# Kernel tuning notes

Measured on AMD Instinct MI355X. Metric: run time of the kernel, lower is better.

The kernel has to match this reference:

```python
import jax, jax.numpy as jnp
import numpy as np

N_NODES = 100000


def _gcn_conv(h, src, dst, norm, W, b):
    # h: [N, F_in] -> [N, F_out]; aggregate normalized messages over edges
    h = h @ W                                   # transform first (cheaper messages)
    msg = h[src] * norm[:, None]                # [E_tot, F_out]
    agg = jax.ops.segment_sum(msg, dst, num_segments=N_NODES)
    return agg + b


def setup_inputs() -> dict:
    key = jax.random.key(0)
    k1, k2, k3, k4 = jax.random.split(key, 4)
    x = jax.random.normal(k1, (N_NODES, 256), dtype=jnp.float32)
    edge_index = jax.random.randint(k2, (2, 1600000), 0, N_NODES, dtype=jnp.int64)
    W1 = jax.random.normal(k3, (256, 128), dtype=jnp.float32) * (1.0 / np.sqrt(256))
    b1 = jnp.zeros((128,), dtype=jnp.float32)
    W2 = jax.random.normal(k4, (128, 40), dtype=jnp.float32) * (1.0 / np.sqrt(128))
    b2 = jnp.zeros((40,), dtype=jnp.float32)
    return {"x": x, "edge_index": edge_index, "W1": W1, "b1": b1, "W2": W2, "b2": b2}


def reference(x, edge_index, W1, b1, W2, b2):
    # add self-loops
    loop = jnp.arange(N_NODES, dtype=edge_index.dtype)
    src = jnp.concatenate([edge_index[0], loop])
    dst = jnp.concatenate([edge_index[1], loop])
    # symmetric normalization D^{-1/2} (A+I) D^{-1/2}
    deg = jax.ops.segment_sum(jnp.ones_like(dst, dtype=x.dtype), dst, num_segments=N_NODES)
    dinv = jax.lax.rsqrt(jnp.maximum(deg, 1.0))
    norm = dinv[src] * dinv[dst]                # [E_tot]

    h = _gcn_conv(x, src, dst, norm, W1, b1)
    h = jax.nn.relu(h)                          # dropout p=0 / eval -> identity
    h = _gcn_conv(h, src, dst, norm, W2, b2)
    return jax.nn.log_softmax(h, axis=1)
```

## Files before the change

### kernel.cpp

```cpp
#include <hip/hip_runtime.h>
#include <hip/hip_fp8.h>
#include <math.h>

#define N_NODES 100000
#define N_EDGES 1600000
#define F_IN 256
#define F_H 128
#define F_OUT 40

#define BIN_SHIFT 9
#define BIN_NODES 512
#define NBIN 196
#define CAP 12288
#define CNT_PAD 16
#define PART_CHUNK 8192

typedef __attribute__((ext_vector_type(8))) short bf16x8;
typedef __attribute__((ext_vector_type(4))) float floatx4;
typedef __attribute__((ext_vector_type(2))) float floatx2;
typedef __attribute__((ext_vector_type(2))) unsigned int uintx2;

__device__ __forceinline__ unsigned short f2bf(float f) {
    unsigned int u = __float_as_uint(f);
    u += 0x7fffu + ((u >> 16) & 1u);
    return (unsigned short)(u >> 16);
}
__device__ __forceinline__ float bf2f(unsigned short s) { return __uint_as_float(((unsigned int)s) << 16); }

#if defined(__has_builtin)
#if __has_builtin(__builtin_amdgcn_cvt_pk_fp8_f32)
#define HAVE_PK_ENC 1
#endif
#if __has_builtin(__builtin_amdgcn_cvt_pk_f32_fp8)
#define HAVE_PK_DEC 1
#endif
#if __has_builtin(__builtin_amdgcn_cvt_f32_fp8)
#define HAVE_SC_DEC 1
#endif
#endif

__device__ __forceinline__ unsigned char f2f8(float f) {
#ifdef HAVE_PK_ENC
    int r = __builtin_amdgcn_cvt_pk_fp8_f32(f, f, 0, false);
    return (unsigned char)(r & 0xff);
#else
    __hip_fp8_e4m3 t(f);
    return (unsigned char)t.__x;
#endif
}
__device__ __forceinline__ float f82f(unsigned char b) {
#ifdef HAVE_SC_DEC
    return __builtin_amdgcn_cvt_f32_fp8((int)b, 0);
#else
    __hip_fp8_e4m3 t; t.__x = (__hip_fp8_storage_t)b;
    return (float)t;
#endif
}
__device__ __forceinline__ floatx2 f8x2tof(unsigned short u) {
#ifdef HAVE_PK_DEC
    return __builtin_amdgcn_cvt_pk_f32_fp8((int)u, false);
#else
    floatx2 r;
    r.x = f82f((unsigned char)(u & 0xff));
    r.y = f82f((unsigned char)(u >> 8));
    return r;
#endif
}

__global__ void k_zero(int* p, int n) {
    int i = blockIdx.x * blockDim.x + threadIdx.x;
    if (i < n) p[i] = 0;
}

__global__ __launch_bounds__(256) void k_part(const int* __restrict__ eidx,
                                              int* __restrict__ gcnt,
                                              unsigned int* __restrict__ parts) {
    __shared__ int hist[4][NBIN];
    __shared__ int sbase[NBIN];
    __shared__ int rcnt[NBIN];
    const int tid = threadIdx.x;
    const int wv = tid >> 6;
    for (int i = tid; i < NBIN; i += 256) {
        hist[0][i] = 0; hist[1][i] = 0; hist[2][i] = 0; hist[3][i] = 0; rcnt[i] = 0;
    }
    __syncthreads();
    const int e0 = blockIdx.x * PART_CHUNK;
    const int e1 = min(e0 + PART_CHUNK, N_EDGES);
    for (int e = e0 + tid; e < e1; e += 256) {
        int d = eidx[N_EDGES + e];
        atomicAdd(&hist[wv][d >> BIN_SHIFT], 1);
    }
    __syncthreads();
    for (int b = tid; b < NBIN; b += 256) {
        int tot = hist[0][b] + hist[1][b] + hist[2][b] + hist[3][b];
        int old = atomicAdd(&gcnt[b * CNT_PAD], tot);
        sbase[b] = b * CAP + old;
    }
    __syncthreads();
    for (int e = e0 + tid; e < e1; e += 256) {
        int d = eidx[N_EDGES + e];
        int s = eidx[e];
        int b = d >> BIN_SHIFT;
        int r = atomicAdd(&rcnt[b], 1);
        parts[sbase[b] + r] = ((unsigned int)s << BIN_SHIFT) | (unsigned int)(d & (BIN_NODES - 1));
    }
}

__global__ __launch_bounds__(256) void k_build(const unsigned int* __restrict__ parts,
                                               const int* __restrict__ gcnt,
                                               int* __restrict__ rowptr,
                                               float* __restrict__ dinv,
                                               int* __restrict__ csr_src) {
    __shared__ int deg[4][BIN_NODES];
    __shared__ int cur[BIN_NODES];
    __shared__ int scan[256];
    const int tid = threadIdx.x;
    const int wv = tid >> 6;
    const int g = blockIdx.x;

    scan[tid] = (tid < NBIN) ? gcnt[tid * CNT_PAD] : 0;
    __syncthreads();
    for (int off = 1; off < 256; off <<= 1) {
        int v = 0;
        if (tid >= off) v = scan[tid - off];
        __syncthreads();
        if (tid >= off) scan[tid] += v;
        __syncthreads();
    }
    const int binBase = (g == 0) ? 0 : scan[g - 1];
    const int cntg = scan[g] - binBase;

    for (int i = tid; i < BIN_NODES; i += 256) {
        deg[0][i] = 0; deg[1][i] = 0; deg[2][i] = 0; deg[3][i] = 0;
    }
    __syncthreads();

    const unsigned int* pp = parts + (size_t)g * CAP;
    for (int i = tid; i < cntg; i += 256)
        atomicAdd(&deg[wv][pp[i] & (BIN_NODES - 1)], 1);
    __syncthreads();

    const int n0 = 2 * tid, n1 = 2 * tid + 1;
    const int d0 = deg[0][n0] + deg[1][n0] + deg[2][n0] + deg[3][n0];
    const int d1 = deg[0][n1] + deg[1][n1] + deg[2][n1] + deg[3][n1];
    scan[tid] = d0 + d1;
    __syncthreads();
    for (int off = 1; off < 256; off <<= 1) {
        int v = 0;
        if (tid >= off) v = scan[tid - off];
        __syncthreads();
        if (tid >= off) scan[tid] += v;
        __syncthreads();
    }
    const int pre = (tid == 0) ? 0 : scan[tid - 1];
    const int p0 = binBase + pre;
    const int p1 = p0 + d0;
    const int node0 = g * BIN_NODES + n0;
    if (node0 < N_NODES)     { rowptr[node0]     = p0; dinv[node0]     = rsqrtf((float)d0 + 1.0f); }
    if (node0 + 1 < N_NODES) { rowptr[node0 + 1] = p1; dinv[node0 + 1] = rsqrtf((float)d1 + 1.0f); }
    cur[n0] = p0;
    cur[n1] = p1;
    __syncthreads();

    for (int i = tid; i < cntg; i += 256) {
        unsigned int u = pp[i];
        int pos = atomicAdd(&cur[u & (BIN_NODES - 1)], 1);
        csr_src[pos] = (int)(u >> BIN_SHIFT);
    }
    if (g == NBIN - 1 && tid == 0) rowptr[N_NODES] = N_EDGES;
}

__global__ void k_cvt_w(const float* __restrict__ W1, const float* __restrict__ W2,
                        short* __restrict__ W1t, short* __restrict__ W2t) {
    int b = blockIdx.x, t = threadIdx.x;
    if (b < 128) {
        int idx = b * 256 + t;
        int n = idx >> 8, k = idx & 255;
        W1t[n * 256 + k] = (short)f2bf(W1[k * 128 + n]);
    } else {
        int idx = (b - 128) * 256 + t;
        if (idx < 48 * 128) {
            int n = idx >> 7, k = idx & 127;
            float v = (n < F_OUT) ? W2[k * F_OUT + n] : 0.f;
            W2t[n * 128 + k] = (short)f2bf(v);
        }
    }
}

__global__ __launch_bounds__(256) void k_gemm1_mfma(const float* __restrict__ x,
                                                    const short* __restrict__ W1t,
                                                    const float* __restrict__ dinv,
                                                    unsigned char* __restrict__ h1f8) {
    __shared__ short As[128 * 40];
    __shared__ short Bs[128 * 264];
    __shared__ float Ds[128];
    const int tid = threadIdx.x;
    const int row0 = blockIdx.x * 128;
    const int w = tid >> 6, l = tid & 63;
    const int l15 = l & 15, q = l >> 4;
    const int ar = tid >> 1;
    const int ak = (tid & 1) * 16;

    {
        const int n = tid >> 1;
        const int kh = (tid & 1) * 128;
#pragma unroll
        for (int i = 0; i < 16; ++i)
            *(bf16x8*)&Bs[n * 264 + kh + i * 8] = *(const bf16x8*)&W1t[n * 256 + kh + i * 8];
    }
    if (tid < 128) {
        int r = row0 + tid;
        Ds[tid] = (r < N_NODES) ? dinv[r] : 0.f;
    }

    floatx4 acc[2][8];
#pragma unroll
    for (int a = 0; a < 2; ++a)
#pragma unroll
        for (int nt = 0; nt < 8; ++nt) acc[a][nt] = (floatx4)0.f;

    const bool arow_ok = (row0 + ar) < N_NODES;
    const float* xp = x + (size_t)(row0 + ar) * F_IN;

    for (int k0 = 0; k0 < F_IN; k0 += 32) {
        bf16x8 av0 = (bf16x8)0, av1 = (bf16x8)0;
        if (arow_ok) {
            floatx4 f0 = *(const floatx4*)(xp + k0 + ak);
            floatx4 f1 = *(const floatx4*)(xp + k0 + ak + 4);
            floatx4 f2 = *(const floatx4*)(xp + k0 + ak + 8);
            floatx4 f3 = *(const floatx4*)(xp + k0 + ak + 12);
            av0[0] = (short)f2bf(f0[0]); av0[1] = (short)f2bf(f0[1]);
            av0[2] = (short)f2bf(f0[2]); av0[3] = (short)f2bf(f0[3]);
            av0[4] = (short)f2bf(f1[0]); av0[5] = (short)f2bf(f1[1]);
            av0[6] = (short)f2bf(f1[2]); av0[7] = (short)f2bf(f1[3]);
            av1[0] = (short)f2bf(f2[0]); av1[1] = (short)f2bf(f2[1]);
            av1[2] = (short)f2bf(f2[2]); av1[3] = (short)f2bf(f2[3]);
            av1[4] = (short)f2bf(f3[0]); av1[5] = (short)f2bf(f3[1]);
            av1[6] = (short)f2bf(f3[2]); av1[7] = (short)f2bf(f3[3]);
        }
        __syncthreads();
        *(bf16x8*)&As[ar * 40 + ak]     = av0;
        *(bf16x8*)&As[ar * 40 + ak + 8] = av1;
        __syncthreads();

        bf16x8 af[2], bfr[8];
#pragma unroll
        for (int a = 0; a < 2; ++a)
            af[a] = *(const bf16x8*)&As[((w * 2 + a) * 16 + l15) * 40 + q * 8];
#pragma unroll
        for (int nt = 0; nt < 8; ++nt)
            bfr[nt] = *(const bf16x8*)&Bs[(nt * 16 + l15) * 264 + k0 + q * 8];
#pragma unroll
        for (int a = 0; a < 2; ++a)
#pragma unroll
            for (int nt = 0; nt < 8; ++nt)
                acc[a][nt] = __builtin_amdgcn_mfma_f32_16x16x32_bf16(af[a], bfr[nt], acc[a][nt], 0, 0, 0);
    }
#pragma unroll
    for (int a = 0; a < 2; ++a) {
#pragma unroll
        for (int r = 0; r < 4; ++r) {
            const int rl = (w * 2 + a) * 16 + q * 4 + r;
            const int row = row0 + rl;
            if (row < N_NODES) {
                const float ds = Ds[rl];
                unsigned char* hp = h1f8 + (size_t)row * F_H;
#pragma unroll
                for (int nt = 0; nt < 8; ++nt)
                    hp[nt * 16 + l15] = f2f8(acc[a][nt][r] * ds);
            }
        }
    }
}

__global__ __launch_bounds__(256) void k_spmm1(const int* __restrict__ rowptr,
                                               const int* __restrict__ csr_src,
                                               const unsigned int* __restrict__ h1d,
                                               const float* __restrict__ dinv,
                                               const float* __restrict__ b1,
                                               uintx2* __restrict__ agg1p2) {
    const int half = threadIdx.x >> 5;
    const int p = threadIdx.x & 31;
    int node = blockIdx.x * 8 + half;
    bool valid = node < N_NODES;
    int nd = valid ? node : 0;
    int beg = rowptr[nd];
    int end = valid ? rowptr[nd + 1] : beg;
    float dv = dinv[nd];

    unsigned int su = h1d[(size_t)nd * 32 + p];
    floatx2 s01 = f8x2tof((unsigned short)(su & 0xffffu));
    floatx2 s23 = f8x2tof((unsigned short)(su >> 16));
    float A0 = s01.x, A1 = s01.y, A2 = s23.x, A3 = s23.y;
    float B0 = 0.f, B1 = 0.f, B2 = 0.f, B3 = 0.f;
    float C0 = 0.f, C1 = 0.f, C2 = 0.f, C3 = 0.f;
    float D0 = 0.f, D1 = 0.f, D2 = 0.f, D3 = 0.f;

    int i = beg;
    for (; i + 3 < end; i += 4) {
        int s0 = csr_src[i], s1 = csr_src[i + 1], s2 = csr_src[i + 2], s3 = csr_src[i + 3];
        unsigned int u0 = h1d[(size_t)s0 * 32 + p];
        unsigned int u1 = h1d[(size_t)s1 * 32 + p];
        unsigned int u2 = h1d[(size_t)s2 * 32 + p];
        unsigned int u3 = h1d[(size_t)s3 * 32 + p];
        floatx2 a01 = f8x2tof((unsigned short)(u0 & 0xffffu));
        floatx2 a23 = f8x2tof((unsigned short)(u0 >> 16));
        floatx2 b01 = f8x2tof((unsigned short)(u1 & 0xffffu));
        floatx2 b23 = f8x2tof((unsigned short)(u1 >> 16));
        floatx2 c01 = f8x2tof((unsigned short)(u2 & 0xffffu));
        floatx2 c23 = f8x2tof((unsigned short)(u2 >> 16));
        floatx2 d01 = f8x2tof((unsigned short)(u3 & 0xffffu));
        floatx2 d23 = f8x2tof((unsigned short)(u3 >> 16));
        A0 += a01.x; A1 += a01.y; A2 += a23.x; A3 += a23.y;
        B0 += b01.x; B1 += b01.y; B2 += b23.x; B3 += b23.y;
        C0 += c01.x; C1 += c01.y; C2 += c23.x; C3 += c23.y;
        D0 += d01.x; D1 += d01.y; D2 += d23.x; D3 += d23.y;
    }
    for (; i < end; ++i) {
        unsigned int u0 = h1d[(size_t)csr_src[i] * 32 + p];
        floatx2 a01 = f8x2tof((unsigned short)(u0 & 0xffffu));
        floatx2 a23 = f8x2tof((unsigned short)(u0 >> 16));
        A0 += a01.x; A1 += a01.y; A2 += a23.x; A3 += a23.y;
    }

    float4 bb = *(const float4*)&b1[4 * p];
    float v0 = fmaf((A0 + B0) + (C0 + D0), dv, bb.x);
    float v1 = fmaf((A1 + B1) + (C1 + D1), dv, bb.y);
    float v2 = fmaf((A2 + B2) + (C2 + D2), dv, bb.z);
    float v3 = fmaf((A3 + B3) + (C3 + D3), dv, bb.w);
    v0 = v0 > 0.f ? v0 : 0.f;
    v1 = v1 > 0.f ? v1 : 0.f;
    v2 = v2 > 0.f ? v2 : 0.f;
    v3 = v3 > 0.f ? v3 : 0.f;
    if (valid) {
        uintx2 o;
        o.x = ((unsigned int)f2bf(v1) << 16) | f2bf(v0);
        o.y = ((unsigned int)f2bf(v3) << 16) | f2bf(v2);
        agg1p2[(size_t)node * 32 + p] = o;
    }
}

__global__ __launch_bounds__(256) void k_gemm2_mfma(const unsigned short* __restrict__ agg1b,
                                                    const short* __restrict__ W2t,
                                                    const float* __restrict__ dinv,
                                                    unsigned char* __restrict__ h2f8) {
    __shared__ short As[128 * 40];
    __shared__ short Bs[48 * 136];
    __shared__ float Ds[128];
    const int tid = threadIdx.x;
    const int row0 = blockIdx.x * 128;
    const int w = tid >> 6, l = tid & 63;
    const int l15 = l & 15, q = l >> 4;
    const int ar = tid >> 1;
    const int ak = (tid & 1) * 16;

#pragma unroll
    for (int i = 0; i < 3; ++i) {
        int c = tid * 3 + i;
        int n = c >> 4, koff = (c & 15) * 8;
        *(bf16x8*)&Bs[n * 136 + koff] = *(const bf16x8*)&W2t[n * 128 + koff];
    }
    if (tid < 128) {
        int r = row0 + tid;
        Ds[tid] = (r < N_NODES) ? dinv[r] : 0.f;
    }

    floatx4 acc[2][3];
#pragma unroll
    for (int a = 0; a < 2; ++a)
#pragma unroll
        for (int nt = 0; nt < 3; ++nt) acc[a][nt] = (floatx4)0.f;

    const bool arow_ok = (row0 + ar) < N_NODES;
    const unsigned short* ap = agg1b + (size_t)(row0 + ar) * F_H;

    for (int k0 = 0; k0 < F_H; k0 += 32) {
        bf16x8 a0, a1;
        if (arow_ok) {
            a0 = *(const bf16x8*)(ap + k0 + ak);
            a1 = *(const bf16x8*)(ap + k0 + ak + 8);
        } else {
            a0 = (bf16x8)0; a1 = (bf16x8)0;
        }
        *(bf16x8*)&As[ar * 40 + ak]     = a0;
        *(bf16x8*)&As[ar * 40 + ak + 8] = a1;
        __syncthreads();

        bf16x8 af[2], bfr[3];
#pragma unroll
        for (int a = 0; a < 2; ++a)
            af[a] = *(const bf16x8*)&As[((w * 2 + a) * 16 + l15) * 40 + q * 8];
#pragma unroll
        for (int nt = 0; nt < 3; ++nt)
            bfr[nt] = *(const bf16x8*)&Bs[(nt * 16 + l15) * 136 + k0 + q * 8];
#pragma unroll
        for (int a = 0; a < 2; ++a)
#pragma unroll
            for (int nt = 0; nt < 3; ++nt)
                acc[a][nt] = __builtin_amdgcn_mfma_f32_16x16x32_bf16(af[a], bfr[nt], acc[a][nt], 0, 0, 0);
        __syncthreads();
    }
#pragma unroll
    for (int a = 0; a < 2; ++a) {
#pragma unroll
        for (int nt = 0; nt < 3; ++nt) {
            int col = nt * 16 + l15;
#pragma unroll
            for (int r = 0; r < 4; ++r) {
                int rl = (w * 2 + a) * 16 + q * 4 + r;
                int row = row0 + rl;
                if (row < N_NODES && col < F_OUT)
                    h2f8[(size_t)row * F_OUT + col] = f2f8(acc[a][nt][r] * Ds[rl]);
            }
        }
    }
}

__global__ __launch_bounds__(256) void k_spmm2_lsm(const int* __restrict__ rowptr,
                                                   const int* __restrict__ csr_src,
                                                   const unsigned int* __restrict__ h2d,
                                                   const float* __restrict__ dinv,
                                                   const float* __restrict__ b2,
                                                   float* __restrict__ out) {
    const int qid = threadIdx.x >> 4;
    const int p = threadIdx.x & 15;
    int node = blockIdx.x * 16 + qid;
    bool nvalid = node < N_NODES;
    bool valid = nvalid && (p < 10);
    int nd = nvalid ? node : 0;
    int beg = 0, end = 0;
    if (valid) { beg = rowptr[nd]; end = rowptr[nd + 1]; }
    float dv = dinv[nd];

    float A0 = 0.f, A1 = 0.f, A2 = 0.f, A3 = 0.f;
    float B0 = 0.f, B1 = 0.f, B2 = 0.f, B3 = 0.f;
    if (valid) {
        unsigned int su = h2d[(size_t)nd * 10 + p];
        floatx2 t0 = f8x2tof((unsigned short)(su & 0xffffu));
        floatx2 t1 = f8x2tof((unsigned short)(su >> 16));
        A0 = t0.x; A1 = t0.y; A2 = t1.x; A3 = t1.y;
    }
    int i = beg;
    for (; i + 1 < end; i += 2) {
        int s0 = csr_src[i], s1 = csr_src[i + 1];
        unsigned int u0 = h2d[(size_t)s0 * 10 + p];
        unsigned int u1 = h2d[(size_t)s1 * 10 + p];
        floatx2 a01 = f8x2tof((unsigned short)(u0 & 0xffffu));
        floatx2 a23 = f8x2tof((unsigned short)(u0 >> 16));
        floatx2 b01 = f8x2tof((unsigned short)(u1 & 0xffffu));
        floatx2 b23 = f8x2tof((unsigned short)(u1 >> 16));
        A0 += a01.x; A1 += a01.y; A2 += a23.x; A3 += a23.y;
        B0 += b01.x; B1 += b01.y; B2 += b23.x; B3 += b23.y;
    }
    if (i < end) {
        unsigned int u0 = h2d[(size_t)csr_src[i] * 10 + p];
        floatx2 a01 = f8x2tof((unsigned short)(u0 & 0xffffu));
        floatx2 a23 = f8x2tof((unsigned short)(u0 >> 16));
        A0 += a01.x; A1 += a01.y; A2 += a23.x; A3 += a23.y;
    }

    float v0 = -INFINITY, v1 = -INFINITY, v2 = -INFINITY, v3 = -INFINITY;
    if (valid) {
        float4 bb = *(const float4*)&b2[4 * p];
        v0 = fmaf(A0 + B0, dv, bb.x);
        v1 = fmaf(A1 + B1, dv, bb.y);
        v2 = fmaf(A2 + B2, dv, bb.z);
        v3 = fmaf(A3 + B3, dv, bb.w);
    }
    float m = fmaxf(fmaxf(v0, v1), fmaxf(v2, v3));
#pragma unroll
    for (int off = 1; off < 16; off <<= 1) m = fmaxf(m, __shfl_xor(m, off, 16));
    float e = 0.f;
    if (valid) e = expf(v0 - m) + expf(v1 - m) + expf(v2 - m) + expf(v3 - m);
#pragma unroll
    for (int off = 1; off < 16; off <<= 1) e += __shfl_xor(e, off, 16);
    if (valid) {
        float ls = logf(e);
        floatx4 o;
        o[0] = v0 - m - ls; o[1] = v1 - m - ls; o[2] = v2 - m - ls; o[3] = v3 - m - ls;
        __builtin_nontemporal_store(o, (floatx4*)&out[(size_t)node * F_OUT + 4 * p]);
    }
}

extern "C" void kernel_launch(void* const* d_in, const int* in_sizes, int n_in,
                              void* d_out, int out_size, void* d_ws, size_t ws_size,
                              hipStream_t stream) {
    const float* x = (const float*)d_in[0];
    const int* eidx = (const int*)d_in[1];
    const float* W1 = (const float*)d_in[2];
    const float* b1 = (const float*)d_in[3];
    const float* W2 = (const float*)d_in[4];
    const float* b2 = (const float*)d_in[5];
    float* out = (float*)d_out;

    char* ws = (char*)d_ws;
    int*   gcnt      = (int*)  (ws);
    int*   rowptr    = (int*)  (ws + 400512);
    int*   csr_src   = (int*)  (ws + 1200528);
    float* dinv      = (float*)(ws + 7600528);
    short* W1t       = (short*)(ws + 8000528);
    short* W2t       = (short*)(ws + 8066064);
    unsigned char*  h1f8  = (unsigned char*) (ws + 8078352);
    unsigned short* agg1b = (unsigned short*)(ws + 20878352);
    unsigned int*   parts = (unsigned int*)  (ws + 20878352);
    unsigned char*  h2f8  = (unsigned char*) (ws + 46478352);

    k_zero<<<(NBIN * CNT_PAD + 255) / 256, 256, 0, stream>>>(gcnt, NBIN * CNT_PAD);
    k_part<<<(N_EDGES + PART_CHUNK - 1) / PART_CHUNK, 256, 0, stream>>>(eidx, gcnt, parts);
    k_build<<<NBIN, 256, 0, stream>>>(parts, gcnt, rowptr, dinv, csr_src);

    k_cvt_w<<<152, 256, 0, stream>>>(W1, W2, W1t, W2t);

    k_gemm1_mfma<<<(N_NODES + 127) / 128, 256, 0, stream>>>(x, W1t, dinv, h1f8);
    k_spmm1<<<(N_NODES + 7) / 8, 256, 0, stream>>>(rowptr, csr_src,
                                                   (const unsigned int*)h1f8, dinv, b1,
                                                   (uintx2*)agg1b);
    k_gemm2_mfma<<<(N_NODES + 127) / 128, 256, 0, stream>>>(agg1b, W2t, dinv, h2f8);
    k_spmm2_lsm<<<(N_NODES + 15) / 16, 256, 0, stream>>>(rowptr, csr_src,
                                                         (const unsigned int*)h2f8, dinv, b2, out);
}
```

Baseline: 339.7 us.

## Widen SpMM1 gathers to 16-byte loads and remap blocks for XCD locality

k_spmm1 now uses 8 lanes per node, each loading 16 fp8 features as one 128-bit vector, in place of 32 lanes loading 4 bytes each. Outputs are written as two 128-bit stores. Block IDs in both k_spmm1 and k_gemm2 are remapped so that consecutive node ranges go to the same XCD (blockIdx mod 8), which should improve L2 reuse between dependent kernels. Each thread now holds 32 accumulators, which raises register pressure, and the remap hardcodes the grid sizes and N_NODES.

```diff
diff --git a/kernel.cpp b/kernel.cpp
--- a/kernel.cpp
+++ b/kernel.cpp
@@ -19,6 +19,7 @@
 typedef __attribute__((ext_vector_type(4))) float floatx4;
 typedef __attribute__((ext_vector_type(2))) float floatx2;
 typedef __attribute__((ext_vector_type(2))) unsigned int uintx2;
+typedef __attribute__((ext_vector_type(4))) unsigned int uintx4;
 
 __device__ __forceinline__ unsigned short f2bf(float f) {
     unsigned int u = __float_as_uint(f);
@@ -65,6 +66,16 @@
     r.y = f82f((unsigned char)(u >> 8));
     return r;
 #endif
+}
+
+__device__ __forceinline__ void acc16(uintx4 u, float* a) {
+#pragma unroll
+    for (int d = 0; d < 4; ++d) {
+        floatx2 lo = f8x2tof((unsigned short)(u[d] & 0xffffu));
+        floatx2 hi = f8x2tof((unsigned short)(u[d] >> 16));
+        a[d * 4 + 0] += lo.x; a[d * 4 + 1] += lo.y;
+        a[d * 4 + 2] += hi.x; a[d * 4 + 3] += hi.y;
+    }
 }
 
 __global__ void k_zero(int* p, int n) {
@@ -275,69 +286,55 @@
 
 __global__ __launch_bounds__(256) void k_spmm1(const int* __restrict__ rowptr,
                                                const int* __restrict__ csr_src,
-                                               const unsigned int* __restrict__ h1d,
+                                               const uintx4* __restrict__ h1d4,
                                                const float* __restrict__ dinv,
                                                const float* __restrict__ b1,
-                                               uintx2* __restrict__ agg1p2) {
-    const int half = threadIdx.x >> 5;
-    const int p = threadIdx.x & 31;
-    int node = blockIdx.x * 8 + half;
-    bool valid = node < N_NODES;
-    int nd = valid ? node : 0;
-    int beg = rowptr[nd];
-    int end = valid ? rowptr[nd + 1] : beg;
-    float dv = dinv[nd];
-
-    unsigned int su = h1d[(size_t)nd * 32 + p];
-    floatx2 s01 = f8x2tof((unsigned short)(su & 0xffffu));
-    floatx2 s23 = f8x2tof((unsigned short)(su >> 16));
-    float A0 = s01.x, A1 = s01.y, A2 = s23.x, A3 = s23.y;
-    float B0 = 0.f, B1 = 0.f, B2 = 0.f, B3 = 0.f;
-    float C0 = 0.f, C1 = 0.f, C2 = 0.f, C3 = 0.f;
-    float D0 = 0.f, D1 = 0.f, D2 = 0.f, D3 = 0.f;
+                                               unsigned short* __restrict__ agg1b) {
+    const int slot = threadIdx.x >> 3;
+    const int p = threadIdx.x & 7;
+    const int bid = blockIdx.x;
+    const int k = bid & 7, j = bid >> 3;
+    const int nb = (k < 5) ? (k * 391 + j) : (5 * 391 + (k - 5) * 390 + j);
+    const int node = nb * 32 + slot;
+
+    const int beg = rowptr[node];
+    const int end = rowptr[node + 1];
+    const float dv = dinv[node];
+
+    float accA[16], accB[16];
+#pragma unroll
+    for (int jj = 0; jj < 16; ++jj) { accA[jj] = 0.f; accB[jj] = 0.f; }
+    acc16(h1d4[(size_t)node * 8 + p], accA);
 
     int i = beg;
     for (; i + 3 < end; i += 4) {
         int s0 = csr_src[i], s1 = csr_src[i + 1], s2 = csr_src[i + 2], s3 = csr_src[i + 3];
-        unsigned int u0 = h1d[(size_t)s0 * 32 + p];
-        unsigned int u1 = h1d[(size_t)s1 * 32 + p];
-        unsigned int u2 = h1d[(size_t)s2 * 32 + p];
-        unsigned int u3 = h1d[(size_t)s3 * 32 + p];
-        floatx2 a01 = f8x2tof((unsigned short)(u0 & 0xffffu));
-        floatx2 a23 = f8x2tof((unsigned short)(u0 >> 16));
-        floatx2 b01 = f8x2tof((unsigned short)(u1 & 0xffffu));
-        floatx2 b23 = f8x2tof((unsigned short)(u1 >> 16));
-        floatx2 c01 = f8x2tof((unsigned short)(u2 & 0xffffu));
-        floatx2 c23 = f8x2tof((unsigned short)(u2 >> 16));
-        floatx2 d01 = f8x2tof((unsigned short)(u3 & 0xffffu));
-        floatx2 d23 = f8x2tof((unsigned short)(u3 >> 16));
-        A0 += a01.x; A1 += a01.y; A2 += a23.x; A3 += a23.y;
-        B0 += b01.x; B1 += b01.y; B2 += b23.x; B3 += b23.y;
-        C0 += c01.x; C1 += c01.y; C2 += c23.x; C3 += c23.y;
-        D0 += d01.x; D1 += d01.y; D2 += d23.x; D3 += d23.y;
-    }
-    for (; i < end; ++i) {
-        unsigned int u0 = h1d[(size_t)csr_src[i] * 32 + p];
-        floatx2 a01 = f8x2tof((unsigned short)(u0 & 0xffffu));
-        floatx2 a23 = f8x2tof((unsigned short)(u0 >> 16));
-        A0 += a01.x; A1 += a01.y; A2 += a23.x; A3 += a23.y;
-    }
-
-    float4 bb = *(const float4*)&b1[4 * p];
-    float v0 = fmaf((A0 + B0) + (C0 + D0), dv, bb.x);
-    float v1 = fmaf((A1 + B1) + (C1 + D1), dv, bb.y);
-    float v2 = fmaf((A2 + B2) + (C2 + D2), dv, bb.z);
-    float v3 = fmaf((A3 + B3) + (C3 + D3), dv, bb.w);
-    v0 = v0 > 0.f ? v0 : 0.f;
-    v1 = v1 > 0.f ? v1 : 0.f;
-    v2 = v2 > 0.f ? v2 : 0.f;
-    v3 = v3 > 0.f ? v3 : 0.f;
-    if (valid) {
-        uintx2 o;
-        o.x = ((unsigned int)f2bf(v1) << 16) | f2bf(v0);
-        o.y = ((unsigned int)f2bf(v3) << 16) | f2bf(v2);
-        agg1p2[(size_t)node * 32 + p] = o;
-    }
+        uintx4 u0 = h1d4[(size_t)s0 * 8 + p];
+        uintx4 u1 = h1d4[(size_t)s1 * 8 + p];
+        uintx4 u2 = h1d4[(size_t)s2 * 8 + p];
+        uintx4 u3 = h1d4[(size_t)s3 * 8 + p];
+        acc16(u0, accA); acc16(u1, accB);
+        acc16(u2, accA); acc16(u3, accB);
+    }
+    for (; i < end; ++i)
+        acc16(h1d4[(size_t)csr_src[i] * 8 + p], accA);
+
+    const float* bp = b1 + 16 * p;
+    unsigned int ow[8];
+#pragma unroll
+    for (int jj = 0; jj < 8; ++jj) {
+        float v0 = fmaf(accA[2 * jj]     + accB[2 * jj],     dv, bp[2 * jj]);
+        float v1 = fmaf(accA[2 * jj + 1] + accB[2 * jj + 1], dv, bp[2 * jj + 1]);
+        v0 = v0 > 0.f ? v0 : 0.f;
+        v1 = v1 > 0.f ? v1 : 0.f;
+        ow[jj] = ((unsigned int)f2bf(v1) << 16) | f2bf(v0);
+    }
+    uintx4* op = (uintx4*)(agg1b + (size_t)node * F_H) + 2 * p;
+    uintx4 o0, o1;
+    o0[0] = ow[0]; o0[1] = ow[1]; o0[2] = ow[2]; o0[3] = ow[3];
+    o1[0] = ow[4]; o1[1] = ow[5]; o1[2] = ow[6]; o1[3] = ow[7];
+    op[0] = o0;
+    op[1] = o1;
 }
 
 __global__ __launch_bounds__(256) void k_gemm2_mfma(const unsigned short* __restrict__ agg1b,
@@ -348,7 +345,10 @@
     __shared__ short Bs[48 * 136];
     __shared__ float Ds[128];
     const int tid = threadIdx.x;
-    const int row0 = blockIdx.x * 128;
+    const int bidr = blockIdx.x;
+    const int kx = bidr & 7, jx = bidr >> 3;
+    const int cb = (kx < 6) ? (kx * 98 + jx) : (6 * 98 + (kx - 6) * 97 + jx);
+    const int row0 = cb * 128;
     const int w = tid >> 6, l = tid & 63;
     const int l15 = l & 15, q = l >> 4;
     const int ar = tid >> 1;
@@ -512,10 +512,9 @@
     k_cvt_w<<<152, 256, 0, stream>>>(W1, W2, W1t, W2t);
 
     k_gemm1_mfma<<<(N_NODES + 127) / 128, 256, 0, stream>>>(x, W1t, dinv, h1f8);
-    k_spmm1<<<(N_NODES + 7) / 8, 256, 0, stream>>>(rowptr, csr_src,
-                                                   (const unsigned int*)h1f8, dinv, b1,
-                                                   (uintx2*)agg1b);
-    k_gemm2_mfma<<<(N_NODES + 127) / 128, 256, 0, stream>>>(agg1b, W2t, dinv, h2f8);
+    k_spmm1<<<3125, 256, 0, stream>>>(rowptr, csr_src,
+                                      (const uintx4*)h1f8, dinv, b1, agg1b);
+    k_gemm2_mfma<<<782, 256, 0, stream>>>(agg1b, W2t, dinv, h2f8);
     k_spmm2_lsm<<<(N_NODES + 15) / 16, 256, 0, stream>>>(rowptr, csr_src,
                                                          (const unsigned int*)h2f8, dinv, b2, out);
 }
```

Result: no change. 335.3 us (-1.3%).
